# Kernel tuning notes

Hardware: AMD Instinct MI355X
Metric: run time of the kernel (lower is better)

The kernel has to match this reference:

```python
import jax, jax.numpy as jnp
import numpy as np

D_MODEL, D_FF, RANK = 1024, 4096, 128
BATCH, SEQ = 4, 2048


def setup_inputs() -> dict:
    key = jax.random.key(0)
    ks = jax.random.split(key, 9)
    s = 0.02  # typical transformer init scale
    return {
        "x": jax.random.normal(ks[0], (BATCH, SEQ, D_MODEL), jnp.float32),
        "cfc_U": jax.random.normal(ks[1], (D_MODEL, RANK), jnp.float32) * s,
        "cfc_S": jax.random.uniform(ks[2], (RANK,), jnp.float32, 0.5, 1.5),
        "cfc_V": jax.random.normal(ks[3], (D_FF, RANK), jnp.float32) * s,
        "cfc_bias": jax.random.normal(ks[4], (D_FF,), jnp.float32) * s,
        "cproj_U": jax.random.normal(ks[5], (D_FF, RANK), jnp.float32) * s,
        "cproj_S": jax.random.uniform(ks[6], (RANK,), jnp.float32, 0.5, 1.5),
        "cproj_V": jax.random.normal(ks[7], (D_MODEL, RANK), jnp.float32) * s,
        "cproj_bias": jax.random.normal(ks[8], (D_MODEL,), jnp.float32) * s,
    }


def reference(x, cfc_U, cfc_S, cfc_V, cfc_bias, cproj_U, cproj_S, cproj_V, cproj_bias):
    # c_fc_weight = (U * S) @ V^T  -> [d_model, d_ff];  h = x @ c_fc_weight + b
    cfc_w = (cfc_U * cfc_S[None, :]) @ cfc_V.T            # [D_MODEL, D_FF]
    h = jnp.einsum('bsd,df->bsf', x, cfc_w) + cfc_bias    # [B, S, D_FF]
    h = jax.nn.gelu(h, approximate=False)                 # nn.GELU() = exact erf
    cproj_w = (cproj_U * cproj_S[None, :]) @ cproj_V.T    # [D_FF, D_MODEL]
    out = jnp.einsum('bsf,fd->bsd', h, cproj_w) + cproj_bias
    return out
```

## Files before the change

kernel.cpp:

```cpp
#include <hip/hip_runtime.h>
#include <math.h>

#define D_MODEL 1024
#define D_FF    4096
#define RANK    128
#define M_ROWS  8192

typedef _Float16 f16;
typedef _Float16 f16x8 __attribute__((ext_vector_type(8)));
typedef float    f32x4 __attribute__((ext_vector_type(4)));

#define MFMA16(a, b, c) __builtin_amdgcn_mfma_f32_16x16x32_f16((a), (b), (c), 0, 0, 0)

__device__ __forceinline__ f16x8 ld8(const f16* p) { return *(const f16x8*)p; }

__device__ __forceinline__ f16x8 cvt8(float4 a0, float4 a1) {
    f16x8 r = { (f16)a0.x, (f16)a0.y, (f16)a0.z, (f16)a0.w,
                (f16)a1.x, (f16)a1.y, (f16)a1.z, (f16)a1.w };
    return r;
}

__device__ __forceinline__ float gelu_fast(float v) {
    float u  = v * 0.70710678118654752440f;
    float au = fabsf(u);
    float t  = __builtin_amdgcn_rcpf(__builtin_fmaf(0.3275911f, au, 1.0f));
    float e  = __expf(-au * au);
    float p  = __builtin_fmaf(1.061405429f, t, -1.453152027f);
    p = __builtin_fmaf(p, t, 1.421413741f);
    p = __builtin_fmaf(p, t, -0.284496736f);
    p = __builtin_fmaf(p, t, 0.254829592f);
    float er = __builtin_fmaf(-p * t, e, 1.0f);
    er = copysignf(er, u);
    return 0.5f * v * (1.0f + er);
}

#define GLOAD16(gp, lp) __builtin_amdgcn_global_load_lds(                     \
    (const __attribute__((address_space(1))) void*)(gp),                      \
    (__attribute__((address_space(3))) void*)(lp), 16, 0, 0)

__global__ __launch_bounds__(256) void k_prep(
    const float* __restrict__ cfcU, const float* __restrict__ cfcS,
    const float* __restrict__ cfcV, const float* __restrict__ pjU,
    const float* __restrict__ pjS,  const float* __restrict__ pjV,
    f16* __restrict__ w1T, f16* __restrict__ v1,
    f16* __restrict__ w2T, f16* __restrict__ v2)
{
    int i = blockIdx.x * 256 + threadIdx.x;
    if (i < 131072) {
        int r = i >> 10, d = i & 1023;
        w1T[i] = (f16)(cfcU[d * RANK + r] * cfcS[r]);
    } else if (i < 655360) {
        int j = i - 131072;
        v1[j] = (f16)cfcV[j];
    } else if (i < 1179648) {
        int j = i - 655360;
        int r = j >> 12, f = j & 4095;
        w2T[j] = (f16)(pjU[f * RANK + r] * pjS[r]);
    } else if (i < 1310720) {
        int j = i - 1179648;
        v2[j] = (f16)pjV[j];
    }
}

__global__ __launch_bounds__(512, 2) void k_t1(
    const float* __restrict__ x, const f16* __restrict__ w1T,
    f16* __restrict__ t1p)
{
    __shared__ __align__(16) f16 w1s[128 * 520];

    const int tid  = threadIdx.x;
    const int lane = tid & 63;
    const int wv   = tid >> 6;
    const int wm   = wv & 3, wn = wv >> 2;
    const int m0b  = blockIdx.x * 64;
    const int h    = blockIdx.y;
    const int c    = lane & 15, q = lane >> 4;

#define LOADX(dst, kc)                                                          \
    _Pragma("unroll") for (int kb = 0; kb < 4; ++kb) {                          \
        const float* px = &x[(size_t)(m0b + wm * 16 + c) * D_MODEL +            \
                             h * 512 + (kc) * 128 + kb * 32 + q * 8];           \
        dst[kb][0] = *(const float4*)px;                                        \
        dst[kb][1] = *(const float4*)(px + 4); }

#define COMPUTEKC(src, kc)                                                      \
    _Pragma("unroll") for (int kb = 0; kb < 4; ++kb) {                          \
        f16x8 af = cvt8(src[kb][0], src[kb][1]);                                \
        _Pragma("unroll") for (int nt = 0; nt < 4; ++nt) {                      \
            f16x8 bf = *(const f16x8*)                                          \
                &w1s[(wn * 64 + nt * 16 + c) * 520 + (kc) * 128 + kb * 32 + q * 8]; \
            acc[nt] = MFMA16(af, bf, acc[nt]); } }

    float4 xa[4][2], xb[4][2];
    LOADX(xa, 0)

#pragma unroll
    for (int i = 0; i < 16; ++i) {
        int id = i * 512 + tid;
        int rr = id >> 6, k8 = id & 63;
        *(f16x8*)&w1s[rr * 520 + k8 * 8] =
            ld8(w1T + (size_t)rr * D_MODEL + h * 512 + k8 * 8);
    }
    __syncthreads();

    f32x4 acc[4] = {};
    LOADX(xb, 1)
    COMPUTEKC(xa, 0)
    LOADX(xa, 2)
    COMPUTEKC(xb, 1)
    LOADX(xb, 3)
    COMPUTEKC(xa, 2)
    COMPUTEKC(xb, 3)

    f16* o = t1p + (size_t)h * (M_ROWS * RANK);
#pragma unroll
    for (int nt = 0; nt < 4; ++nt)
#pragma unroll
        for (int i2 = 0; i2 < 4; ++i2)
            o[(size_t)(m0b + wm * 16 + q * 4 + i2) * RANK + wn * 64 + nt * 16 + c] =
                (f16)acc[nt][i2];
#undef LOADX
#undef COMPUTEKC
}

#define V1OFF 0
#define W2OFF 32768
#define HSOFF 65536
#define HSTR  56

__global__ __launch_bounds__(256, 2) void k_fused(
    const f16* __restrict__ t1p, const f16* __restrict__ v1,
    const float* __restrict__ bfc, const f16* __restrict__ w2T,
    f16* __restrict__ t2p)
{
    __shared__ __align__(16) char smem[72704];

    const int tid  = threadIdx.x;
    const int lane = tid & 63;
    const int wv   = tid >> 6;
    const int wm   = wv & 1, wf = wv >> 1;
    const int c    = lane & 15, q = lane >> 4;

    const int bx  = blockIdx.x;
    const int s   = (bx & 7) >> 2;
    const int mb  = (bx >> 3) * 4 + (bx & 3);
    const int m0b = mb * 32;
    const int fw  = wf * 32;

    f16* hsw = (f16*)(smem + HSOFF + wv * (16 * HSTR * 2));

#define STAGE(bsel, itn) {                                                      \
    const int ft_ = s * 2048 + (itn) * 64;                                      \
    _Pragma("unroll") for (int i = 0; i < 4; ++i) {                             \
        int rb_  = wv * 16 + i * 4;                                             \
        int row_ = rb_ + (lane >> 4);                                           \
        int col_ = ((lane & 15) * 16) ^ ((row_ & 7) << 4);                      \
        GLOAD16((const char*)v1 + (size_t)(ft_ + row_) * 256 + col_,            \
                smem + V1OFF + (bsel) * 16384 + rb_ * 256);                     \
    }                                                                           \
    _Pragma("unroll") for (int i = 0; i < 4; ++i) {                             \
        int rb_  = wv * 32 + i * 8;                                             \
        int row_ = rb_ + (lane >> 3);                                           \
        int col_ = ((lane & 7) * 16) ^ ((row_ & 7) << 4);                       \
        GLOAD16((const char*)w2T + (size_t)row_ * 8192 + (size_t)ft_ * 2 + col_,\
                smem + W2OFF + (bsel) * 16384 + rb_ * 128);                     \
    }                                                                           \
}

    f16x8 a2[4];
#pragma unroll
    for (int kb = 0; kb < 4; ++kb) {
        const size_t off = (size_t)(m0b + wm * 16 + c) * RANK + kb * 32 + q * 8;
        f16x8 p0 = ld8(t1p + off);
        f16x8 p1 = ld8(t1p + (size_t)(M_ROWS * RANK) + off);
#pragma unroll
        for (int e = 0; e < 8; ++e)
            a2[kb][e] = (f16)((float)p0[e] + (float)p1[e]);
    }

    STAGE(0, 0)
    __syncthreads();

    f32x4 c3[8] = {};

#pragma unroll 1
    for (int it = 0; it < 32; ++it) {
        const int cur = it & 1;
        const int ft  = s * 2048 + it * 64;

        float bb[2];
        bb[0] = bfc[ft + fw + c];
        bb[1] = bfc[ft + fw + 16 + c];

        if (it < 31) STAGE(cur ^ 1, it + 1)

        f32x4 c2[2] = {};
#pragma unroll
        for (int nt = 0; nt < 2; ++nt)
#pragma unroll
            for (int kb = 0; kb < 4; ++kb) {
                int row = fw + nt * 16 + c;
                f16x8 bv = *(const f16x8*)(smem + V1OFF + cur * 16384 +
                    row * 256 + ((kb * 64 + q * 16) ^ ((row & 7) << 4)));
                c2[nt] = MFMA16(a2[kb], bv, c2[nt]);
            }

#pragma unroll
        for (int nt = 0; nt < 2; ++nt)
#pragma unroll
            for (int i2 = 0; i2 < 4; ++i2)
                hsw[(q * 4 + i2) * HSTR + nt * 16 + c] =
                    (f16)gelu_fast(c2[nt][i2] + bb[nt]);
        asm volatile("s_waitcnt lgkmcnt(0)" ::: "memory");

        f16x8 a3 = *(const f16x8*)(hsw + c * HSTR + q * 8);
#pragma unroll
        for (int rt = 0; rt < 8; ++rt) {
            int rr = rt * 16 + c;
            f16x8 bw = *(const f16x8*)(smem + W2OFF + cur * 16384 +
                rr * 128 + ((wf * 64 + q * 16) ^ ((c & 7) << 4)));
            c3[rt] = MFMA16(a3, bw, c3[rt]);
        }
        asm volatile("s_waitcnt lgkmcnt(0)" ::: "memory");

        __syncthreads();
    }
#undef STAGE

    float* rbuf = (float*)smem;

    if (wf == 1) {
        float* rb = rbuf + wm * 2112;
#pragma unroll
        for (int rt = 0; rt < 8; ++rt)
#pragma unroll
            for (int i2 = 0; i2 < 4; ++i2)
                rb[(q * 4 + i2) * 132 + rt * 16 + c] = c3[rt][i2];
    }
    __syncthreads();
    if (wf == 0) {
        float* rb = rbuf + wm * 2112;
#pragma unroll
        for (int rt = 0; rt < 8; ++rt)
#pragma unroll
            for (int i2 = 0; i2 < 4; ++i2)
                c3[rt][i2] += rb[(q * 4 + i2) * 132 + rt * 16 + c];
        f16* o = t2p + (size_t)s * (M_ROWS * RANK);
#pragma unroll
        for (int rt = 0; rt < 8; ++rt)
#pragma unroll
            for (int i2 = 0; i2 < 4; ++i2)
                o[(size_t)(m0b + wm * 16 + q * 4 + i2) * RANK + rt * 16 + c] =
                    (f16)c3[rt][i2];
    }
}

__global__ __launch_bounds__(256, 2) void k_out(
    const f16* __restrict__ t2p, const f16* __restrict__ v2,
    const float* __restrict__ bpj, float* __restrict__ out)
{
    __shared__ __align__(16) f16 v2s[256 * 136];

    const int tid  = threadIdx.x;
    const int lane = tid & 63;
    const int wv   = tid >> 6;
    const int wm   = wv & 1, wn = wv >> 1;
    const int m0b  = blockIdx.x * 32;
    const int n0b  = blockIdx.y * 256;
    const int c    = lane & 15, q = lane >> 4;

#pragma unroll
    for (int i8 = 0; i8 < 16; ++i8) {
        int id = i8 * 256 + tid;
        int nn = id >> 4, k8 = id & 15;
        *(f16x8*)&v2s[nn * 136 + k8 * 8] =
            ld8(v2 + (size_t)(n0b + nn) * RANK + k8 * 8);
    }

    f16x8 a[4];
#pragma unroll
    for (int kb = 0; kb < 4; ++kb) {
        const size_t off = (size_t)(m0b + wm * 16 + c) * RANK + kb * 32 + q * 8;
        f16x8 p0 = ld8(t2p + off);
        f16x8 p1 = ld8(t2p + (size_t)(M_ROWS * RANK) + off);
#pragma unroll
        for (int e = 0; e < 8; ++e)
            a[kb][e] = (f16)((float)p0[e] + (float)p1[e]);
    }
    __syncthreads();

    f32x4 acc[8] = {};
#pragma unroll
    for (int nt = 0; nt < 8; ++nt)
#pragma unroll
        for (int kb = 0; kb < 4; ++kb) {
            f16x8 bf = *(const f16x8*)
                &v2s[(wn * 128 + nt * 16 + c) * 136 + kb * 32 + q * 8];
            acc[nt] = MFMA16(a[kb], bf, acc[nt]);
        }

#pragma unroll
    for (int nt = 0; nt < 8; ++nt) {
        float b = bpj[n0b + wn * 128 + nt * 16 + c];
#pragma unroll
        for (int i2 = 0; i2 < 4; ++i2)
            out[(size_t)(m0b + wm * 16 + q * 4 + i2) * D_MODEL +
                n0b + wn * 128 + nt * 16 + c] = acc[nt][i2] + b;
    }
}

extern "C" void kernel_launch(void* const* d_in, const int* in_sizes, int n_in,
                              void* d_out, int out_size, void* d_ws, size_t ws_size,
                              hipStream_t stream) {
    const float* x    = (const float*)d_in[0];
    const float* cfcU = (const float*)d_in[1];
    const float* cfcS = (const float*)d_in[2];
    const float* cfcV = (const float*)d_in[3];
    const float* cfcB = (const float*)d_in[4];
    const float* pjU  = (const float*)d_in[5];
    const float* pjS  = (const float*)d_in[6];
    const float* pjV  = (const float*)d_in[7];
    const float* pjB  = (const float*)d_in[8];
    float* out = (float*)d_out;

    f16* wsf = (f16*)d_ws;
    f16* t1p = wsf;
    f16* t2p = wsf + 2097152;
    f16* w1T = wsf + 4194304;
    f16* v1  = w1T + 131072;
    f16* w2T = v1  + 524288;
    f16* v2  = w2T + 524288;

    k_prep <<<dim3(5120), 256, 0, stream>>>(cfcU, cfcS, cfcV, pjU, pjS, pjV,
                                            w1T, v1, w2T, v2);
    k_t1   <<<dim3(M_ROWS / 64, 2), 512, 0, stream>>>(x, w1T, t1p);
    k_fused<<<dim3(512), 256, 0, stream>>>(t1p, v1, cfcB, w2T, t2p);
    k_out  <<<dim3(M_ROWS / 32, D_MODEL / 256), 256, 0, stream>>>(t2p, v2, pjB, out);
}
```

Measured before the change: 167.5 us.

## Tile-transpose weight prep, async-stage swizzled W1 in k_t1, widen k_out blocks

k_prep now transposes U*S through a shared-memory tile with coalesced float4 reads and vector f16 writes, and converts V with 8-wide vectors. This replaces the old strided scalar gather. k_t1 shrinks to 256-thread, 32-row blocks and stages W1 in two K halves with global_load_lds into an XOR-swizzled LDS buffer, halving its shared-memory footprint. k_out goes to 512 threads and 64 rows per block, so each V2 tile load is reused across more rows. The extra barriers and smaller k_t1 tiles add sync overhead and reload W1 more often.

```diff
diff --git a/kernel.cpp b/kernel.cpp
--- a/kernel.cpp
+++ b/kernel.cpp
@@ -8,6 +8,7 @@
 
 typedef _Float16 f16;
 typedef _Float16 f16x8 __attribute__((ext_vector_type(8)));
+typedef _Float16 f16x4 __attribute__((ext_vector_type(4)));
 typedef float    f32x4 __attribute__((ext_vector_type(4)));
 
 #define MFMA16(a, b, c) __builtin_amdgcn_mfma_f32_16x16x32_f16((a), (b), (c), 0, 0, 0)
@@ -45,36 +46,62 @@
     f16* __restrict__ w1T, f16* __restrict__ v1,
     f16* __restrict__ w2T, f16* __restrict__ v2)
 {
-    int i = blockIdx.x * 256 + threadIdx.x;
-    if (i < 131072) {
-        int r = i >> 10, d = i & 1023;
-        w1T[i] = (f16)(cfcU[d * RANK + r] * cfcS[r]);
-    } else if (i < 655360) {
-        int j = i - 131072;
-        v1[j] = (f16)cfcV[j];
-    } else if (i < 1179648) {
-        int j = i - 655360;
-        int r = j >> 12, f = j & 4095;
-        w2T[j] = (f16)(pjU[f * RANK + r] * pjS[r]);
-    } else if (i < 1310720) {
-        int j = i - 1179648;
-        v2[j] = (f16)pjV[j];
-    }
-}
-
-__global__ __launch_bounds__(512, 2) void k_t1(
+    __shared__ float tile[32][33];
+    const int b = blockIdx.x, t = threadIdx.x;
+
+    if (b < 320) {
+        int j = (b * 256 + t) * 8;
+        const float* src; f16* dst;
+        if (j < 524288) { src = cfcV + j;            dst = v1 + j; }
+        else            { src = pjV + (j - 524288);  dst = v2 + (j - 524288); }
+        float4 a0 = *(const float4*)src, a1 = *(const float4*)(src + 4);
+        *(f16x8*)dst = cvt8(a0, a1);
+        return;
+    }
+
+    const float* src; const float* S; f16* dst; int R, tb;
+    if (b < 448) { src = cfcU; S = cfcS; dst = w1T; R = 1024; tb = b - 320; }
+    else         { src = pjU;  S = pjS;  dst = w2T; R = 4096; tb = b - 448; }
+    const int td = tb >> 2, tr = tb & 3;
+
+    const int r0 = t >> 3, c0 = (t & 7) * 4;
+    float4 v  = *(const float4*)(src + (size_t)(td * 32 + r0) * 128 + tr * 32 + c0);
+    float4 sv = *(const float4*)(S + tr * 32 + c0);
+    tile[r0][c0 + 0] = v.x * sv.x;
+    tile[r0][c0 + 1] = v.y * sv.y;
+    tile[r0][c0 + 2] = v.z * sv.z;
+    tile[r0][c0 + 3] = v.w * sv.w;
+    __syncthreads();
+
+    const int j = t >> 3, i4 = (t & 7) * 4;
+    f16x4 o = { (f16)tile[i4 + 0][j], (f16)tile[i4 + 1][j],
+                (f16)tile[i4 + 2][j], (f16)tile[i4 + 3][j] };
+    *(f16x4*)&dst[(size_t)(tr * 32 + j) * R + td * 32 + i4] = o;
+}
+
+__global__ __launch_bounds__(256, 2) void k_t1(
     const float* __restrict__ x, const f16* __restrict__ w1T,
     f16* __restrict__ t1p)
 {
-    __shared__ __align__(16) f16 w1s[128 * 520];
+    __shared__ __align__(16) char w1s[65536];
 
     const int tid  = threadIdx.x;
     const int lane = tid & 63;
     const int wv   = tid >> 6;
-    const int wm   = wv & 3, wn = wv >> 2;
-    const int m0b  = blockIdx.x * 64;
+    const int wm   = wv & 1, wn = wv >> 1;
+    const int m0b  = blockIdx.x * 32;
     const int h    = blockIdx.y;
     const int c    = lane & 15, q = lane >> 4;
+
+#define STAGEW(kk)                                                              \
+    _Pragma("unroll") for (int i = 0; i < 16; ++i) {                            \
+        int r0_  = wv * 32 + i * 2;                                             \
+        int row_ = r0_ + (lane >> 5);                                           \
+        int col_ = ((lane & 31) * 16) ^ ((row_ & 7) << 4);                      \
+        GLOAD16((const char*)w1T + (size_t)row_ * 2048 + h * 1024 +             \
+                (kk) * 512 + col_,                                              \
+                w1s + r0_ * 512);                                               \
+    }
 
 #define LOADX(dst, kc)                                                          \
     _Pragma("unroll") for (int kb = 0; kb < 4; ++kb) {                          \
@@ -83,34 +110,31 @@
         dst[kb][0] = *(const float4*)px;                                        \
         dst[kb][1] = *(const float4*)(px + 4); }
 
-#define COMPUTEKC(src, kc)                                                      \
+#define COMPUTEKC(src, sc)                                                      \
     _Pragma("unroll") for (int kb = 0; kb < 4; ++kb) {                          \
         f16x8 af = cvt8(src[kb][0], src[kb][1]);                                \
         _Pragma("unroll") for (int nt = 0; nt < 4; ++nt) {                      \
-            f16x8 bf = *(const f16x8*)                                          \
-                &w1s[(wn * 64 + nt * 16 + c) * 520 + (kc) * 128 + kb * 32 + q * 8]; \
+            int row_ = wn * 64 + nt * 16 + c;                                   \
+            f16x8 bf = *(const f16x8*)(w1s + row_ * 512 +                       \
+                (((sc) * 256 + kb * 64 + q * 16) ^ ((row_ & 7) << 4)));         \
             acc[nt] = MFMA16(af, bf, acc[nt]); } }
 
     float4 xa[4][2], xb[4][2];
     LOADX(xa, 0)
-
-#pragma unroll
-    for (int i = 0; i < 16; ++i) {
-        int id = i * 512 + tid;
-        int rr = id >> 6, k8 = id & 63;
-        *(f16x8*)&w1s[rr * 520 + k8 * 8] =
-            ld8(w1T + (size_t)rr * D_MODEL + h * 512 + k8 * 8);
-    }
+    STAGEW(0)
     __syncthreads();
 
     f32x4 acc[4] = {};
     LOADX(xb, 1)
     COMPUTEKC(xa, 0)
+    COMPUTEKC(xb, 1)
+    __syncthreads();
+    STAGEW(1)
     LOADX(xa, 2)
+    __syncthreads();
+    LOADX(xb, 3)
+    COMPUTEKC(xa, 0)
     COMPUTEKC(xb, 1)
-    LOADX(xb, 3)
-    COMPUTEKC(xa, 2)
-    COMPUTEKC(xb, 3)
 
     f16* o = t1p + (size_t)h * (M_ROWS * RANK);
 #pragma unroll
@@ -119,6 +143,7 @@
         for (int i2 = 0; i2 < 4; ++i2)
             o[(size_t)(m0b + wm * 16 + q * 4 + i2) * RANK + wn * 64 + nt * 16 + c] =
                 (f16)acc[nt][i2];
+#undef STAGEW
 #undef LOADX
 #undef COMPUTEKC
 }
@@ -255,7 +280,7 @@
     }
 }
 
-__global__ __launch_bounds__(256, 2) void k_out(
+__global__ __launch_bounds__(512, 2) void k_out(
     const f16* __restrict__ t2p, const f16* __restrict__ v2,
     const float* __restrict__ bpj, float* __restrict__ out)
 {
@@ -264,14 +289,14 @@
     const int tid  = threadIdx.x;
     const int lane = tid & 63;
     const int wv   = tid >> 6;
-    const int wm   = wv & 1, wn = wv >> 1;
-    const int m0b  = blockIdx.x * 32;
+    const int wm   = wv & 3, wn = wv >> 2;
+    const int m0b  = blockIdx.x * 64;
     const int n0b  = blockIdx.y * 256;
     const int c    = lane & 15, q = lane >> 4;
 
 #pragma unroll
-    for (int i8 = 0; i8 < 16; ++i8) {
-        int id = i8 * 256 + tid;
+    for (int i8 = 0; i8 < 8; ++i8) {
+        int id = i8 * 512 + tid;
         int nn = id >> 4, k8 = id & 15;
         *(f16x8*)&v2s[nn * 136 + k8 * 8] =
             ld8(v2 + (size_t)(n0b + nn) * RANK + k8 * 8);
@@ -331,9 +356,9 @@
     f16* w2T = v1  + 524288;
     f16* v2  = w2T + 524288;
 
-    k_prep <<<dim3(5120), 256, 0, stream>>>(cfcU, cfcS, cfcV, pjU, pjS, pjV,
-                                            w1T, v1, w2T, v2);
-    k_t1   <<<dim3(M_ROWS / 64, 2), 512, 0, stream>>>(x, w1T, t1p);
+    k_prep <<<dim3(960), 256, 0, stream>>>(cfcU, cfcS, cfcV, pjU, pjS, pjV,
+                                           w1T, v1, w2T, v2);
+    k_t1   <<<dim3(M_ROWS / 32, 2), 256, 0, stream>>>(x, w1T, t1p);
     k_fused<<<dim3(512), 256, 0, stream>>>(t1p, v1, cfcB, w2T, t2p);
-    k_out  <<<dim3(M_ROWS / 32, D_MODEL / 256), 256, 0, stream>>>(t2p, v2, pjB, out);
-}
+    k_out  <<<dim3(M_ROWS / 64, D_MODEL / 256), 512, 0, stream>>>(t2p, v2, pjB, out);
+}
```

Result: no change. 167.1 us (-0.2%).
